# Performance work log

Hardware: AMD Instinct MI355X
Metric: run time of the kernel (lower is better)

## Reference

```python
import jax, jax.numpy as jnp
import numpy as np

D_MODEL = 1024
N_HEADS = 16
HEAD_DIM = 64  # 'hidden' per head; n_heads*hidden == d_model


def setup_inputs() -> dict:
    key = jax.random.key(0)
    ks = jax.random.split(key, 11)
    B, S = 4, 2048
    scale = 1.0 / np.sqrt(D_MODEL)
    return {
        "query": jax.random.normal(ks[0], (B, S, D_MODEL), jnp.float32),
        "key": jax.random.normal(ks[1], (B, S, D_MODEL), jnp.float32),
        "value": jax.random.normal(ks[2], (B, S, D_MODEL), jnp.float32),
        "Wq": jax.random.normal(ks[3], (D_MODEL, N_HEADS * HEAD_DIM), jnp.float32) * scale,
        "bq": jnp.zeros((N_HEADS * HEAD_DIM,), jnp.float32),
        "Wk": jax.random.normal(ks[4], (D_MODEL, N_HEADS * HEAD_DIM), jnp.float32) * scale,
        "bk": jnp.zeros((N_HEADS * HEAD_DIM,), jnp.float32),
        "Wv": jax.random.normal(ks[5], (D_MODEL, N_HEADS * HEAD_DIM), jnp.float32) * scale,
        "bv": jnp.zeros((N_HEADS * HEAD_DIM,), jnp.float32),
        "Wo": jax.random.normal(ks[6], (N_HEADS * HEAD_DIM, D_MODEL), jnp.float32) * scale,
        "bo": jnp.zeros((D_MODEL,), jnp.float32),
    }


def reference(query, key, value, Wq, bq, Wk, bk, Wv, bv, Wo, bo):
    B, Sq, _ = query.shape
    Sk = key.shape[1]
    # QKV projections -> [B, H, S, d]
    q = (query @ Wq + bq).reshape(B, Sq, N_HEADS, HEAD_DIM).transpose(0, 2, 1, 3)
    k = (key @ Wk + bk).reshape(B, Sk, N_HEADS, HEAD_DIM).transpose(0, 2, 1, 3)
    v = (value @ Wv + bv).reshape(B, Sk, N_HEADS, HEAD_DIM).transpose(0, 2, 1, 3)
    # scores [B, H, Sq, Sk]
    scores = jnp.einsum("bhqd,bhkd->bhqk", q, k) / np.sqrt(HEAD_DIM).astype(np.float32)
    probs = jax.nn.softmax(scores, axis=-1)  # dropout: identity (eval mode)
    z = jnp.einsum("bhqk,bhkd->bhqd", probs, v)
    z = z.transpose(0, 2, 1, 3).reshape(B, Sq, N_HEADS * HEAD_DIM)
    return z @ Wo + bo
```

## Files before the change

### kernel.cpp

```cpp
#include <hip/hip_runtime.h>
#include <hip/hip_bf16.h>

typedef unsigned short ushort_t;
typedef unsigned int u32;
typedef __attribute__((ext_vector_type(8))) short short8;
typedef short8 __attribute__((may_alias)) short8_ma;
typedef __attribute__((ext_vector_type(4))) float f32x4;
typedef f32x4 __attribute__((may_alias)) f32x4_ma;
typedef __attribute__((ext_vector_type(2))) unsigned int u32x2;
typedef u32x2 __attribute__((may_alias)) u32x2_ma;
typedef __attribute__((ext_vector_type(4))) unsigned int u32x4;
typedef u32x4 __attribute__((may_alias)) u32x4_ma;

#if __has_builtin(__builtin_amdgcn_exp2f)
#define EXP2(x) __builtin_amdgcn_exp2f(x)
#else
#define EXP2(x) exp2f(x)
#endif

__device__ __forceinline__ unsigned short f2bf(float f) {
    union { float f; unsigned int i; } x; x.f = f;
    unsigned int r = x.i + 0x7FFFu + ((x.i >> 16) & 1u);
    return (unsigned short)(r >> 16);
}
__device__ __forceinline__ unsigned int bfround(float f) {
    union { float f; unsigned int i; } x; x.f = f;
    return x.i + 0x7FFFu + ((x.i >> 16) & 1u);
}
__device__ __forceinline__ unsigned int pack2bf(float lo, float hi) {
    return __builtin_amdgcn_perm(bfround(hi), bfround(lo), 0x07060302u);
}
__device__ __forceinline__ u32 cvtpk_bf16(float lo, float hi) {
    u32 r;
    asm("v_cvt_pk_bf16_f32 %0, %1, %2" : "=v"(r) : "v"(lo), "v"(hi));
    return r;
}
__device__ __forceinline__ f32x4 mfma16x16x32(short8 a, short8 b, f32x4 c) {
    return __builtin_amdgcn_mfma_f32_16x16x32_bf16(a, b, c, 0, 0, 0);
}
typedef const __attribute__((address_space(1))) u32 gu32;
typedef __attribute__((address_space(3))) u32 lu32;
__device__ __forceinline__ void async16(const ushort_t* g, ushort_t* l) {
    __builtin_amdgcn_global_load_lds((gu32*)g, (lu32*)l, 16, 0, 0);
}

__global__ __launch_bounds__(256)
void cast3(const float* __restrict__ A0, const float* __restrict__ A1,
           const float* __restrict__ A2, ushort_t* __restrict__ O0,
           ushort_t* __restrict__ O1, ushort_t* __restrict__ O2) {
    const float* A; ushort_t* O;
    switch (blockIdx.z) {
        case 0: A = A0; O = O0; break;
        case 1: A = A1; O = O1; break;
        default: A = A2; O = O2; break;
    }
    size_t idx = ((size_t)blockIdx.x * 256 + threadIdx.x) * 8;
    f32x4 v0 = *(const f32x4_ma*)(A + idx);
    f32x4 v1 = *(const f32x4_ma*)(A + idx + 4);
    u32x4 pk;
    pk[0] = pack2bf(v0[0], v0[1]);
    pk[1] = pack2bf(v0[2], v0[3]);
    pk[2] = pack2bf(v1[0], v1[1]);
    pk[3] = pack2bf(v1[2], v1[3]);
    *(u32x4_ma*)(O + idx) = pk;
}

__global__ __launch_bounds__(256)
void transpose4(const float* __restrict__ W0, const float* __restrict__ W1,
                const float* __restrict__ W2, const float* __restrict__ W3,
                ushort_t* __restrict__ T0, ushort_t* __restrict__ T1,
                ushort_t* __restrict__ T2, ushort_t* __restrict__ T3) {
    __shared__ ushort_t tile[64][65];
    const float* W; ushort_t* T;
    switch (blockIdx.z) {
        case 0: W = W0; T = T0; break;
        case 1: W = W1; T = T1; break;
        case 2: W = W2; T = T2; break;
        default: W = W3; T = T3; break;
    }
    int bx = blockIdx.x * 64, by = blockIdx.y * 64;
    int tx = threadIdx.x & 63, ty = threadIdx.x >> 6;
    #pragma unroll
    for (int i = 0; i < 64; i += 4)
        tile[ty + i][tx] = f2bf(W[(size_t)(by + ty + i) * 1024 + bx + tx]);
    __syncthreads();
    #pragma unroll
    for (int i = 0; i < 64; i += 4)
        T[(size_t)(bx + ty + i) * 1024 + by + tx] = tile[tx][ty + i];
}

__global__ __launch_bounds__(256)
void vtrans(const ushort_t* __restrict__ V, ushort_t* __restrict__ VtG) {
    __shared__ ushort_t tile[64][65];
    int kt = blockIdx.x;
    int bh = blockIdx.y;
    int b = bh >> 4, h = bh & 15;
    int tx = threadIdx.x & 63, ty = threadIdx.x >> 6;
    #pragma unroll
    for (int i = 0; i < 64; i += 4)
        tile[ty + i][tx] = V[(size_t)(b * 2048 + kt * 64 + ty + i) * 1024 + h * 64 + tx];
    __syncthreads();
    #pragma unroll
    for (int i = 0; i < 64; i += 4)
        VtG[((size_t)bh * 64 + ty + i) * 2048 + kt * 64 + tx] = tile[tx][ty + i];
}

template<bool C_F32>
__global__ __launch_bounds__(256)
void gemm_async(const ushort_t* __restrict__ A, const ushort_t* __restrict__ Bt,
                const float* __restrict__ bias, void* __restrict__ Cab,
                int M, int N, int K, float outscale) {
    __shared__ __align__(16) ushort_t As[2][128 * 64];
    __shared__ __align__(16) ushort_t Bs[2][128 * 64];
    const int t = threadIdx.x;
    const int m0 = blockIdx.y * 128, n0 = blockIdx.x * 128;
    const int w = t >> 6, lane = t & 63, quad = lane >> 4, lr = lane & 15;
    const int wm = (w >> 1) * 64, wn = (w & 1) * 64;
    const int lrow8 = lane >> 3, lchunk = lane & 7;
    const int sw = (lchunk ^ lrow8) * 8;

    f32x4 acc[4][4] = {};

    #pragma unroll
    for (int i = 0; i < 4; i++) {
        int ra = 32 * w + 8 * i + lrow8;
        async16(A  + (size_t)(m0 + ra) * K + sw, &As[0][(32 * w + 8 * i) * 64]);
        async16(Bt + (size_t)(n0 + ra) * K + sw, &Bs[0][(32 * w + 8 * i) * 64]);
    }

    int cur = 0;
    for (int k0 = 0; k0 < K; k0 += 64) {
        __syncthreads();
        if (k0 + 64 < K) {
            int nxt = cur ^ 1;
            #pragma unroll
            for (int i = 0; i < 4; i++) {
                int ra = 32 * w + 8 * i + lrow8;
                async16(A  + (size_t)(m0 + ra) * K + k0 + 64 + sw, &As[nxt][(32 * w + 8 * i) * 64]);
                async16(Bt + (size_t)(n0 + ra) * K + k0 + 64 + sw, &Bs[nxt][(32 * w + 8 * i) * 64]);
            }
        }
        #pragma unroll
        for (int kc = 0; kc < 2; kc++) {
            short8 af[4], bf[4];
            int pa = ((4 * kc + quad) ^ (lr & 7)) * 8;
            #pragma unroll
            for (int i = 0; i < 4; i++) {
                af[i] = *(const short8_ma*)(As[cur] + (wm + i * 16 + lr) * 64 + pa);
                bf[i] = *(const short8_ma*)(Bs[cur] + (wn + i * 16 + lr) * 64 + pa);
            }
            #pragma unroll
            for (int i = 0; i < 4; i++)
                #pragma unroll
                for (int j = 0; j < 4; j++)
                    acc[i][j] = mfma16x16x32(af[i], bf[j], acc[i][j]);
        }
        cur ^= 1;
    }

    #pragma unroll
    for (int i = 0; i < 4; i++) {
        int row = m0 + wm + i * 16 + quad * 4;
        #pragma unroll
        for (int j = 0; j < 4; j++) {
            int col = n0 + wn + j * 16 + lr;
            float bv = bias[col];
            #pragma unroll
            for (int r = 0; r < 4; r++) {
                size_t idx = (size_t)(row + r) * N + col;
                if (C_F32) ((float*)Cab)[idx] = acc[i][j][r] + bv;
                else ((ushort_t*)Cab)[idx] = f2bf((acc[i][j][r] + bv) * outscale);
            }
        }
    }
}

__global__ __launch_bounds__(256)
void attn_fwd(const ushort_t* __restrict__ Q, const ushort_t* __restrict__ Kg,
              const ushort_t* __restrict__ VtG, ushort_t* __restrict__ Z) {
    __shared__ __align__(16) ushort_t Ks[2][64 * 64];
    __shared__ __align__(16) ushort_t Vt[2][64 * 64];
    __shared__ __align__(16) ushort_t Pt[128 * 64];

    const int t = threadIdx.x;
    const int qt = blockIdx.x;
    const int bh = blockIdx.y;
    const int b = bh >> 4, h = bh & 15;
    const int w = t >> 6, lane = t & 63, quad = lane >> 4, lr = lane & 15;
    const int lrow8 = lane >> 3, lchunk = lane & 7;

    const size_t rs = 1024;
    const size_t qbase = ((size_t)b * 2048 + qt * 128) * rs + h * 64;
    const size_t kvbase = ((size_t)b * 2048) * rs + h * 64;
    const size_t vbase = (size_t)bh * 64 * 2048;

    short8 qf[2][2];
    #pragma unroll
    for (int mt = 0; mt < 2; mt++)
        #pragma unroll
        for (int kc = 0; kc < 2; kc++)
            qf[mt][kc] = *(const short8_ma*)(Q + qbase + (size_t)(w * 32 + mt * 16 + lr) * rs + kc * 32 + quad * 8);

    f32x4 oacc[2][4] = {};
    float mrow[2] = { -INFINITY, -INFINITY };
    float lrow[2] = { 0.f, 0.f };

    const int rloc0 = 16 * w + lrow8;
    const int sw = (lchunk ^ lrow8) * 8;

    #pragma unroll
    for (int i = 0; i < 2; i++) {
        int rloc = rloc0 + 8 * i;
        async16(Kg + kvbase + (size_t)rloc * rs + sw, &Ks[0][(16 * w + 8 * i) * 64]);
        async16(VtG + vbase + (size_t)rloc * 2048 + sw, &Vt[0][(16 * w + 8 * i) * 64]);
    }

    int cur = 0;
    for (int kt = 0; kt < 32; kt++) {
        __syncthreads();
        if (kt < 31) {
            int nxt = cur ^ 1;
            #pragma unroll
            for (int i = 0; i < 2; i++) {
                int rloc = rloc0 + 8 * i;
                async16(Kg + kvbase + (size_t)((kt + 1) * 64 + rloc) * rs + sw, &Ks[nxt][(16 * w + 8 * i) * 64]);
                async16(VtG + vbase + (size_t)rloc * 2048 + (kt + 1) * 64 + sw, &Vt[nxt][(16 * w + 8 * i) * 64]);
            }
        }
        const ushort_t* Kc = Ks[cur];
        const ushort_t* Vc = Vt[cur];

        f32x4 sacc[4][2] = {};
        #pragma unroll
        for (int kc = 0; kc < 2; kc++) {
            short8 kf[4];
            int pa = ((4 * kc + quad) ^ (lr & 7)) * 8;
            #pragma unroll
            for (int nt = 0; nt < 4; nt++)
                kf[nt] = *(const short8_ma*)(Kc + (nt * 16 + lr) * 64 + pa);
            #pragma unroll
            for (int nt = 0; nt < 4; nt++)
                #pragma unroll
                for (int mt = 0; mt < 2; mt++)
                    sacc[nt][mt] = mfma16x16x32(kf[nt], qf[mt][kc], sacc[nt][mt]);
        }

        #pragma unroll
        for (int mt = 0; mt < 2; mt++) {
            float a0 = fmaxf(fmaxf(sacc[0][mt][0], sacc[0][mt][1]), sacc[0][mt][2]);
            float a1 = fmaxf(fmaxf(sacc[0][mt][3], sacc[1][mt][0]), sacc[1][mt][1]);
            float a2 = fmaxf(fmaxf(sacc[1][mt][2], sacc[1][mt][3]), sacc[2][mt][0]);
            float a3 = fmaxf(fmaxf(sacc[2][mt][1], sacc[2][mt][2]), sacc[2][mt][3]);
            float a4 = fmaxf(fmaxf(sacc[3][mt][0], sacc[3][mt][1]), sacc[3][mt][2]);
            float b0 = fmaxf(fmaxf(a0, a1), a2);
            float b1 = fmaxf(fmaxf(a3, a4), sacc[3][mt][3]);
            float mx = fmaxf(b0, b1);
            mx = fmaxf(mx, __shfl_xor(mx, 16, 64));
            mx = fmaxf(mx, __shfl_xor(mx, 32, 64));

            if (!__all(mx <= mrow[mt] + 8.0f)) {
                float mnew = fmaxf(mrow[mt], mx);
                float alpha = EXP2(mrow[mt] - mnew);
                mrow[mt] = mnew;
                lrow[mt] *= alpha;
                oacc[mt][0] *= alpha;
                oacc[mt][1] *= alpha;
                oacc[mt][2] *= alpha;
                oacc[mt][3] *= alpha;
            }
            const float mcur = mrow[mt];

            float rsum = 0.f;
            const int prow = w * 32 + mt * 16 + lr;
            #pragma unroll
            for (int nt = 0; nt < 4; nt++) {
                float p0 = EXP2(sacc[nt][mt][0] - mcur);
                float p1 = EXP2(sacc[nt][mt][1] - mcur);
                float p2 = EXP2(sacc[nt][mt][2] - mcur);
                float p3 = EXP2(sacc[nt][mt][3] - mcur);
                rsum += (p0 + p1) + (p2 + p3);
                u32x2 pw;
                pw[0] = cvtpk_bf16(p0, p1);
                pw[1] = cvtpk_bf16(p2, p3);
                int phys = (2 * nt + (quad >> 1)) ^ (lr & 7);
                *(u32x2_ma*)(Pt + prow * 64 + phys * 8 + (quad & 1) * 4) = pw;
            }
            rsum += __shfl_xor(rsum, 16, 64);
            rsum += __shfl_xor(rsum, 32, 64);
            lrow[mt] += rsum;
        }

        asm volatile("" ::: "memory");

        #pragma unroll
        for (int kc2 = 0; kc2 < 2; kc2++) {
            short8 pf[2], vf[4];
            int pp = ((4 * kc2 + quad) ^ (lr & 7)) * 8;
            #pragma unroll
            for (int mt = 0; mt < 2; mt++)
                pf[mt] = *(const short8_ma*)(Pt + (w * 32 + mt * 16 + lr) * 64 + pp);
            #pragma unroll
            for (int dn = 0; dn < 4; dn++)
                vf[dn] = *(const short8_ma*)(Vc + (dn * 16 + lr) * 64 + pp);
            #pragma unroll
            for (int mt = 0; mt < 2; mt++)
                #pragma unroll
                for (int dn = 0; dn < 4; dn++)
                    oacc[mt][dn] = mfma16x16x32(vf[dn], pf[mt], oacc[mt][dn]);
        }
        cur ^= 1;
    }

    ushort_t* Ot = Pt;
    float inv[2] = { 1.f / lrow[0], 1.f / lrow[1] };
    asm volatile("" ::: "memory");
    #pragma unroll
    for (int mt = 0; mt < 2; mt++)
        #pragma unroll
        for (int dn = 0; dn < 4; dn++) {
            u32x2 pw;
            pw[0] = cvtpk_bf16(oacc[mt][dn][0] * inv[mt], oacc[mt][dn][1] * inv[mt]);
            pw[1] = cvtpk_bf16(oacc[mt][dn][2] * inv[mt], oacc[mt][dn][3] * inv[mt]);
            int phys = (2 * dn + (quad >> 1)) ^ (lr & 7);
            *(u32x2_ma*)(Ot + (w * 32 + mt * 16 + lr) * 64 + phys * 8 + (quad & 1) * 4) = pw;
        }
    asm volatile("" ::: "memory");
    {
        int qrow = t >> 1;
        int dhalf = (t & 1) * 32;
        #pragma unroll
        for (int cc = 0; cc < 4; cc++) {
            int phys = ((4 * (t & 1) + cc) ^ (qrow & 7)) * 8;
            short8 v = *(const short8_ma*)(Ot + qrow * 64 + phys);
            *(short8_ma*)(Z + qbase + (size_t)qrow * rs + dhalf + cc * 8) = v;
        }
    }
}

extern "C" void kernel_launch(void* const* d_in, const int* in_sizes, int n_in,
                              void* d_out, int out_size, void* d_ws, size_t ws_size,
                              hipStream_t stream) {
    const float* query = (const float*)d_in[0];
    const float* key   = (const float*)d_in[1];
    const float* value = (const float*)d_in[2];
    const float* Wq = (const float*)d_in[3];
    const float* bq = (const float*)d_in[4];
    const float* Wk = (const float*)d_in[5];
    const float* bk = (const float*)d_in[6];
    const float* Wv = (const float*)d_in[7];
    const float* bv = (const float*)d_in[8];
    const float* Wo = (const float*)d_in[9];
    const float* bo = (const float*)d_in[10];
    float* out = (float*)d_out;

    char* ws = (char*)d_ws;
    const size_t WSZ = 1024ull * 1024 * 2;
    const size_t QSZ = 8192ull * 1024 * 2;
    const size_t BW = 4 * WSZ;
    ushort_t* WqT = (ushort_t*)(ws + 0 * WSZ);
    ushort_t* WkT = (ushort_t*)(ws + 1 * WSZ);
    ushort_t* WvT = (ushort_t*)(ws + 2 * WSZ);
    ushort_t* WoT = (ushort_t*)(ws + 3 * WSZ);
    ushort_t* S1 = (ushort_t*)(ws + BW + 0 * QSZ);
    ushort_t* S2 = (ushort_t*)(ws + BW + 1 * QSZ);
    ushort_t* S3 = (ushort_t*)(ws + BW + 2 * QSZ);
    ushort_t* S4 = (ushort_t*)(ws + BW + 3 * QSZ);

    cast3<<<dim3(4096, 1, 3), 256, 0, stream>>>(query, key, value, S1, S2, S3);
    transpose4<<<dim3(16, 16, 4), 256, 0, stream>>>(Wq, Wk, Wv, Wo, WqT, WkT, WvT, WoT);

    dim3 gg(8, 64);
    gemm_async<false><<<gg, 256, 0, stream>>>(S1, WqT, bq, S4, 8192, 1024, 1024, 0.125f * 1.4426950408889634f);
    gemm_async<false><<<gg, 256, 0, stream>>>(S2, WkT, bk, S1, 8192, 1024, 1024, 1.0f);
    gemm_async<false><<<gg, 256, 0, stream>>>(S3, WvT, bv, S2, 8192, 1024, 1024, 1.0f);

    vtrans<<<dim3(32, 64), 256, 0, stream>>>(S2, S3);

    attn_fwd<<<dim3(16, 64), 256, 0, stream>>>(S4, S1, S3, S4);

    gemm_async<true><<<gg, 256, 0, stream>>>(S4, WoT, bo, out, 8192, 1024, 1024, 1.0f);
}
```

Baseline: 391.8 us.

## Load GEMM B operand directly to registers and shrink attention P buffer

Measured after the change: 480.0 us. 1.23x slower.

```diff
diff --git a/kernel.cpp b/kernel.cpp
--- a/kernel.cpp
+++ b/kernel.cpp
@@ -105,13 +105,38 @@
         VtG[((size_t)bh * 64 + ty + i) * 2048 + kt * 64 + tx] = tile[tx][ty + i];
 }
 
+__device__ __forceinline__ void loadB(short8 (&b)[2][4], const ushort_t* bp,
+                                      int koff, int K) {
+    #pragma unroll
+    for (int kc = 0; kc < 2; kc++)
+        #pragma unroll
+        for (int j = 0; j < 4; j++)
+            b[kc][j] = *(const short8_ma*)(bp + koff + (size_t)j * 16 * K + kc * 32);
+}
+__device__ __forceinline__ void computeA(f32x4 (&acc)[4][4], const ushort_t* Abuf,
+                                         const short8 (&b)[2][4], int wm, int lr,
+                                         int quad) {
+    #pragma unroll
+    for (int kc = 0; kc < 2; kc++) {
+        short8 af[4];
+        int pa = ((4 * kc + quad) ^ (lr & 7)) * 8;
+        #pragma unroll
+        for (int i = 0; i < 4; i++)
+            af[i] = *(const short8_ma*)(Abuf + (wm + i * 16 + lr) * 64 + pa);
+        #pragma unroll
+        for (int i = 0; i < 4; i++)
+            #pragma unroll
+            for (int j = 0; j < 4; j++)
+                acc[i][j] = mfma16x16x32(af[i], b[kc][j], acc[i][j]);
+    }
+}
+
 template<bool C_F32>
 __global__ __launch_bounds__(256)
-void gemm_async(const ushort_t* __restrict__ A, const ushort_t* __restrict__ Bt,
-                const float* __restrict__ bias, void* __restrict__ Cab,
-                int M, int N, int K, float outscale) {
+void gemm_bd(const ushort_t* __restrict__ A, const ushort_t* __restrict__ Bt,
+             const float* __restrict__ bias, void* __restrict__ Cab,
+             int M, int N, int K, float outscale) {
     __shared__ __align__(16) ushort_t As[2][128 * 64];
-    __shared__ __align__(16) ushort_t Bs[2][128 * 64];
     const int t = threadIdx.x;
     const int m0 = blockIdx.y * 128, n0 = blockIdx.x * 128;
     const int w = t >> 6, lane = t & 63, quad = lane >> 4, lr = lane & 15;
@@ -119,44 +144,34 @@
     const int lrow8 = lane >> 3, lchunk = lane & 7;
     const int sw = (lchunk ^ lrow8) * 8;
 
+    const ushort_t* bp = Bt + (size_t)(n0 + wn + lr) * K + quad * 8;
+
     f32x4 acc[4][4] = {};
-
-    #pragma unroll
-    for (int i = 0; i < 4; i++) {
-        int ra = 32 * w + 8 * i + lrow8;
-        async16(A  + (size_t)(m0 + ra) * K + sw, &As[0][(32 * w + 8 * i) * 64]);
-        async16(Bt + (size_t)(n0 + ra) * K + sw, &Bs[0][(32 * w + 8 * i) * 64]);
-    }
-
-    int cur = 0;
-    for (int k0 = 0; k0 < K; k0 += 64) {
+    short8 b0[2][4], b1[2][4];
+
+    #define STAGEA(dst, koff) do { \
+        _Pragma("unroll") \
+        for (int i_ = 0; i_ < 4; i_++) { \
+            int ra_ = 32 * w + 8 * i_ + lrow8; \
+            async16(A + (size_t)(m0 + ra_) * K + (koff) + sw, &(dst)[(32 * w + 8 * i_) * 64]); \
+        } } while (0)
+
+    STAGEA(As[0], 0);
+    loadB(b0, bp, 0, K);
+
+    for (int k0 = 0; k0 < K; k0 += 128) {
         __syncthreads();
-        if (k0 + 64 < K) {
-            int nxt = cur ^ 1;
-            #pragma unroll
-            for (int i = 0; i < 4; i++) {
-                int ra = 32 * w + 8 * i + lrow8;
-                async16(A  + (size_t)(m0 + ra) * K + k0 + 64 + sw, &As[nxt][(32 * w + 8 * i) * 64]);
-                async16(Bt + (size_t)(n0 + ra) * K + k0 + 64 + sw, &Bs[nxt][(32 * w + 8 * i) * 64]);
-            }
-        }
-        #pragma unroll
-        for (int kc = 0; kc < 2; kc++) {
-            short8 af[4], bf[4];
-            int pa = ((4 * kc + quad) ^ (lr & 7)) * 8;
-            #pragma unroll
-            for (int i = 0; i < 4; i++) {
-                af[i] = *(const short8_ma*)(As[cur] + (wm + i * 16 + lr) * 64 + pa);
-                bf[i] = *(const short8_ma*)(Bs[cur] + (wn + i * 16 + lr) * 64 + pa);
-            }
-            #pragma unroll
-            for (int i = 0; i < 4; i++)
-                #pragma unroll
-                for (int j = 0; j < 4; j++)
-                    acc[i][j] = mfma16x16x32(af[i], bf[j], acc[i][j]);
-        }
-        cur ^= 1;
-    }
+        STAGEA(As[1], k0 + 64);
+        loadB(b1, bp, k0 + 64, K);
+        computeA(acc, As[0], b0, wm, lr, quad);
+        __syncthreads();
+        if (k0 + 128 < K) {
+            STAGEA(As[0], k0 + 128);
+            loadB(b0, bp, k0 + 128, K);
+        }
+        computeA(acc, As[1], b1, wm, lr, quad);
+    }
+    #undef STAGEA
 
     #pragma unroll
     for (int i = 0; i < 4; i++) {
@@ -180,7 +195,7 @@
               const ushort_t* __restrict__ VtG, ushort_t* __restrict__ Z) {
     __shared__ __align__(16) ushort_t Ks[2][64 * 64];
     __shared__ __align__(16) ushort_t Vt[2][64 * 64];
-    __shared__ __align__(16) ushort_t Pt[128 * 64];
+    __shared__ __align__(16) ushort_t Pt64[64 * 64];
 
     const int t = threadIdx.x;
     const int qt = blockIdx.x;
@@ -231,6 +246,7 @@
         const ushort_t* Vc = Vt[cur];
 
         f32x4 sacc[4][2] = {};
+        __builtin_amdgcn_s_setprio(1);
         #pragma unroll
         for (int kc = 0; kc < 2; kc++) {
             short8 kf[4];
@@ -244,6 +260,7 @@
                 for (int mt = 0; mt < 2; mt++)
                     sacc[nt][mt] = mfma16x16x32(kf[nt], qf[mt][kc], sacc[nt][mt]);
         }
+        __builtin_amdgcn_s_setprio(0);
 
         #pragma unroll
         for (int mt = 0; mt < 2; mt++) {
@@ -271,7 +288,7 @@
             const float mcur = mrow[mt];
 
             float rsum = 0.f;
-            const int prow = w * 32 + mt * 16 + lr;
+            const int prow16 = w * 16 + lr;
             #pragma unroll
             for (int nt = 0; nt < 4; nt++) {
                 float p0 = EXP2(sacc[nt][mt][0] - mcur);
@@ -283,37 +300,34 @@
                 pw[0] = cvtpk_bf16(p0, p1);
                 pw[1] = cvtpk_bf16(p2, p3);
                 int phys = (2 * nt + (quad >> 1)) ^ (lr & 7);
-                *(u32x2_ma*)(Pt + prow * 64 + phys * 8 + (quad & 1) * 4) = pw;
+                *(u32x2_ma*)(Pt64 + prow16 * 64 + phys * 8 + (quad & 1) * 4) = pw;
             }
             rsum += __shfl_xor(rsum, 16, 64);
             rsum += __shfl_xor(rsum, 32, 64);
             lrow[mt] += rsum;
-        }
-
-        asm volatile("" ::: "memory");
-
-        #pragma unroll
-        for (int kc2 = 0; kc2 < 2; kc2++) {
-            short8 pf[2], vf[4];
-            int pp = ((4 * kc2 + quad) ^ (lr & 7)) * 8;
-            #pragma unroll
-            for (int mt = 0; mt < 2; mt++)
-                pf[mt] = *(const short8_ma*)(Pt + (w * 32 + mt * 16 + lr) * 64 + pp);
-            #pragma unroll
-            for (int dn = 0; dn < 4; dn++)
-                vf[dn] = *(const short8_ma*)(Vc + (dn * 16 + lr) * 64 + pp);
-            #pragma unroll
-            for (int mt = 0; mt < 2; mt++)
+
+            asm volatile("" ::: "memory");
+
+            __builtin_amdgcn_s_setprio(1);
+            #pragma unroll
+            for (int kc2 = 0; kc2 < 2; kc2++) {
+                int pp = ((4 * kc2 + quad) ^ (lr & 7)) * 8;
+                short8 pf = *(const short8_ma*)(Pt64 + prow16 * 64 + pp);
                 #pragma unroll
-                for (int dn = 0; dn < 4; dn++)
-                    oacc[mt][dn] = mfma16x16x32(vf[dn], pf[mt], oacc[mt][dn]);
+                for (int dn = 0; dn < 4; dn++) {
+                    short8 vf = *(const short8_ma*)(Vc + (dn * 16 + lr) * 64 + pp);
+                    oacc[mt][dn] = mfma16x16x32(vf, pf, oacc[mt][dn]);
+                }
+            }
+            __builtin_amdgcn_s_setprio(0);
+            asm volatile("" ::: "memory");
         }
         cur ^= 1;
     }
 
-    ushort_t* Ot = Pt;
+    __syncthreads();
+    ushort_t* Ot = (ushort_t*)Ks;
     float inv[2] = { 1.f / lrow[0], 1.f / lrow[1] };
-    asm volatile("" ::: "memory");
     #pragma unroll
     for (int mt = 0; mt < 2; mt++)
         #pragma unroll
@@ -370,13 +384,13 @@
     transpose4<<<dim3(16, 16, 4), 256, 0, stream>>>(Wq, Wk, Wv, Wo, WqT, WkT, WvT, WoT);
 
     dim3 gg(8, 64);
-    gemm_async<false><<<gg, 256, 0, stream>>>(S1, WqT, bq, S4, 8192, 1024, 1024, 0.125f * 1.4426950408889634f);
-    gemm_async<false><<<gg, 256, 0, stream>>>(S2, WkT, bk, S1, 8192, 1024, 1024, 1.0f);
-    gemm_async<false><<<gg, 256, 0, stream>>>(S3, WvT, bv, S2, 8192, 1024, 1024, 1.0f);
+    gemm_bd<false><<<gg, 256, 0, stream>>>(S1, WqT, bq, S4, 8192, 1024, 1024, 0.125f * 1.4426950408889634f);
+    gemm_bd<false><<<gg, 256, 0, stream>>>(S2, WkT, bk, S1, 8192, 1024, 1024, 1.0f);
+    gemm_bd<false><<<gg, 256, 0, stream>>>(S3, WvT, bv, S2, 8192, 1024, 1024, 1.0f);
 
     vtrans<<<dim3(32, 64), 256, 0, stream>>>(S2, S3);
 
     attn_fwd<<<dim3(16, 64), 256, 0, stream>>>(S4, S1, S3, S4);
 
-    gemm_async<true><<<gg, 256, 0, stream>>>(S4, WoT, bo, out, 8192, 1024, 1024, 1.0f);
-}
+    gemm_bd<true><<<gg, 256, 0, stream>>>(S4, WoT, bo, out, 8192, 1024, 1024, 1.0f);
+}
```

## Fuse V transpose into V-projection epilogue and remap block indices for XCD locality

Applied to the files above, without the earlier changes.

Result: faster. 377.9 us (-3.5%).

```diff
diff --git a/kernel.cpp b/kernel.cpp
--- a/kernel.cpp
+++ b/kernel.cpp
@@ -89,23 +89,7 @@
         T[(size_t)(bx + ty + i) * 1024 + by + tx] = tile[tx][ty + i];
 }
 
-__global__ __launch_bounds__(256)
-void vtrans(const ushort_t* __restrict__ V, ushort_t* __restrict__ VtG) {
-    __shared__ ushort_t tile[64][65];
-    int kt = blockIdx.x;
-    int bh = blockIdx.y;
-    int b = bh >> 4, h = bh & 15;
-    int tx = threadIdx.x & 63, ty = threadIdx.x >> 6;
-    #pragma unroll
-    for (int i = 0; i < 64; i += 4)
-        tile[ty + i][tx] = V[(size_t)(b * 2048 + kt * 64 + ty + i) * 1024 + h * 64 + tx];
-    __syncthreads();
-    #pragma unroll
-    for (int i = 0; i < 64; i += 4)
-        VtG[((size_t)bh * 64 + ty + i) * 2048 + kt * 64 + tx] = tile[tx][ty + i];
-}
-
-template<bool C_F32>
+template<int MODE>
 __global__ __launch_bounds__(256)
 void gemm_async(const ushort_t* __restrict__ A, const ushort_t* __restrict__ Bt,
                 const float* __restrict__ bias, void* __restrict__ Cab,
@@ -113,7 +97,9 @@
     __shared__ __align__(16) ushort_t As[2][128 * 64];
     __shared__ __align__(16) ushort_t Bs[2][128 * 64];
     const int t = threadIdx.x;
-    const int m0 = blockIdx.y * 128, n0 = blockIdx.x * 128;
+    const int old = blockIdx.x + (blockIdx.y << 3);
+    const int neu = ((old & 7) << 6) | (old >> 3);
+    const int n0 = (neu & 7) * 128, m0 = (neu >> 3) * 128;
     const int w = t >> 6, lane = t & 63, quad = lane >> 4, lr = lane & 15;
     const int wm = (w >> 1) * 64, wn = (w & 1) * 64;
     const int lrow8 = lane >> 3, lchunk = lane & 7;
@@ -121,25 +107,21 @@
 
     f32x4 acc[4][4] = {};
 
-    #pragma unroll
-    for (int i = 0; i < 4; i++) {
-        int ra = 32 * w + 8 * i + lrow8;
-        async16(A  + (size_t)(m0 + ra) * K + sw, &As[0][(32 * w + 8 * i) * 64]);
-        async16(Bt + (size_t)(n0 + ra) * K + sw, &Bs[0][(32 * w + 8 * i) * 64]);
-    }
+    #define STAGEAB(dst, koff) do { \
+        _Pragma("unroll") \
+        for (int i_ = 0; i_ < 4; i_++) { \
+            int ra_ = 32 * w + 8 * i_ + lrow8; \
+            async16(A  + (size_t)(m0 + ra_) * K + (koff) + sw, &As[dst][(32 * w + 8 * i_) * 64]); \
+            async16(Bt + (size_t)(n0 + ra_) * K + (koff) + sw, &Bs[dst][(32 * w + 8 * i_) * 64]); \
+        } } while (0)
+
+    STAGEAB(0, 0);
 
     int cur = 0;
     for (int k0 = 0; k0 < K; k0 += 64) {
         __syncthreads();
-        if (k0 + 64 < K) {
-            int nxt = cur ^ 1;
-            #pragma unroll
-            for (int i = 0; i < 4; i++) {
-                int ra = 32 * w + 8 * i + lrow8;
-                async16(A  + (size_t)(m0 + ra) * K + k0 + 64 + sw, &As[nxt][(32 * w + 8 * i) * 64]);
-                async16(Bt + (size_t)(n0 + ra) * K + k0 + 64 + sw, &Bs[nxt][(32 * w + 8 * i) * 64]);
-            }
-        }
+        if (k0 + 64 < K)
+            STAGEAB(cur ^ 1, k0 + 64);
         #pragma unroll
         for (int kc = 0; kc < 2; kc++) {
             short8 af[4], bf[4];
@@ -157,6 +139,7 @@
         }
         cur ^= 1;
     }
+    #undef STAGEAB
 
     #pragma unroll
     for (int i = 0; i < 4; i++) {
@@ -165,11 +148,19 @@
         for (int j = 0; j < 4; j++) {
             int col = n0 + wn + j * 16 + lr;
             float bv = bias[col];
-            #pragma unroll
-            for (int r = 0; r < 4; r++) {
-                size_t idx = (size_t)(row + r) * N + col;
-                if (C_F32) ((float*)Cab)[idx] = acc[i][j][r] + bv;
-                else ((ushort_t*)Cab)[idx] = f2bf((acc[i][j][r] + bv) * outscale);
+            if (MODE == 2) {
+                u32x2 pw;
+                pw[0] = cvtpk_bf16(acc[i][j][0] + bv, acc[i][j][1] + bv);
+                pw[1] = cvtpk_bf16(acc[i][j][2] + bv, acc[i][j][3] + bv);
+                size_t vrow = (size_t)(((row >> 11) << 4) | (col >> 6)) * 64 + (col & 63);
+                *(u32x2_ma*)((ushort_t*)Cab + vrow * 2048 + (row & 2047)) = pw;
+            } else {
+                #pragma unroll
+                for (int r = 0; r < 4; r++) {
+                    size_t idx = (size_t)(row + r) * N + col;
+                    if (MODE == 1) ((float*)Cab)[idx] = acc[i][j][r] + bv;
+                    else ((ushort_t*)Cab)[idx] = f2bf((acc[i][j][r] + bv) * outscale);
+                }
             }
         }
     }
@@ -183,8 +174,10 @@
     __shared__ __align__(16) ushort_t Pt[128 * 64];
 
     const int t = threadIdx.x;
-    const int qt = blockIdx.x;
-    const int bh = blockIdx.y;
+    const int old = blockIdx.x + (blockIdx.y << 4);
+    const int neu = ((old & 7) << 7) | (old >> 3);
+    const int qt = neu & 15;
+    const int bh = neu >> 4;
     const int b = bh >> 4, h = bh & 15;
     const int w = t >> 6, lane = t & 63, quad = lane >> 4, lr = lane & 15;
     const int lrow8 = lane >> 3, lchunk = lane & 7;
@@ -370,13 +363,11 @@
     transpose4<<<dim3(16, 16, 4), 256, 0, stream>>>(Wq, Wk, Wv, Wo, WqT, WkT, WvT, WoT);
 
     dim3 gg(8, 64);
-    gemm_async<false><<<gg, 256, 0, stream>>>(S1, WqT, bq, S4, 8192, 1024, 1024, 0.125f * 1.4426950408889634f);
-    gemm_async<false><<<gg, 256, 0, stream>>>(S2, WkT, bk, S1, 8192, 1024, 1024, 1.0f);
-    gemm_async<false><<<gg, 256, 0, stream>>>(S3, WvT, bv, S2, 8192, 1024, 1024, 1.0f);
-
-    vtrans<<<dim3(32, 64), 256, 0, stream>>>(S2, S3);
-
-    attn_fwd<<<dim3(16, 64), 256, 0, stream>>>(S4, S1, S3, S4);
-
-    gemm_async<true><<<gg, 256, 0, stream>>>(S4, WoT, bo, out, 8192, 1024, 1024, 1.0f);
-}
+    gemm_async<0><<<gg, 256, 0, stream>>>(S1, WqT, bq, S4, 8192, 1024, 1024, 0.125f * 1.4426950408889634f);
+    gemm_async<0><<<gg, 256, 0, stream>>>(S2, WkT, bk, S1, 8192, 1024, 1024, 1.0f);
+    gemm_async<2><<<gg, 256, 0, stream>>>(S3, WvT, bv, S2, 8192, 1024, 1024, 1.0f);
+
+    attn_fwd<<<dim3(16, 64), 256, 0, stream>>>(S4, S1, S2, S4);
+
+    gemm_async<1><<<gg, 256, 0, stream>>>(S4, WoT, bo, out, 8192, 1024, 1024, 1.0f);
+}
```
